# Kernel tuning notes

Hardware: AMD Instinct MI355X
Metric: run time of the kernel (lower is better)

The kernel has to match this reference:

```python
import jax, jax.numpy as jnp
import numpy as np

K = 16            # number of instance labels (static; labels are 0..K-1)
DELTA_V = 0.2     # delta_variance_loss
DELTA_D = 0.2     # delta_cluster_distance
ALPHA, BETA, GAMMA = 1.0, 1.0, 0.001


def _safe_sqrt(x):
    # sqrt with zero (not nan) gradient at x == 0
    pos = x > 0
    return jnp.where(pos, jnp.sqrt(jnp.where(pos, x, 1.0)), 0.0)


def setup_inputs() -> dict:
    key = jax.random.key(0)
    k1, k2 = jax.random.split(key)
    features = jax.random.normal(k1, (4, 32, 256, 512), dtype=jnp.float32)
    ground_truth = jax.random.randint(k2, (4, 256, 512), 0, K, dtype=jnp.int64)
    return {"features": features, "ground_truth": ground_truth}


def reference(features, ground_truth):
    N, C, H, W = features.shape
    P = H * W
    feat = features.reshape(N, C, P)                  # (N,C,P)
    gt = ground_truth.reshape(N, P)                   # (N,P)
    onehot = (gt[:, :, None] == jnp.arange(K)[None, None, :]).astype(feat.dtype)  # (N,P,K)

    # cluster mean: torch.mean(feature * mask, dim=1) -> masked sum / (H*W)  (faithful quirk)
    mu = jnp.einsum('ncp,npk->nck', feat, onehot) / P  # (N,C,K)

    # ---- variance loss ----
    # per pixel p, instance k: || feat[:,p]*mask_pk - mu[:,k] ||_2 over channels.
    # expand: mask*(||f||^2 - 2 f.mu) + ||mu||^2   (mask in {0,1} so mask^2 = mask)
    sq_f = jnp.sum(feat * feat, axis=1)               # (N,P)
    dot = jnp.einsum('ncp,nck->npk', feat, mu)        # (N,P,K)
    sq_mu = jnp.sum(mu * mu, axis=1)                  # (N,K)
    sq = onehot * (sq_f[:, :, None] - 2.0 * dot) + sq_mu[:, None, :]  # (N,P,K)
    d = _safe_sqrt(jnp.maximum(sq, 0.0))
    v = jnp.mean(d, axis=1)                           # (N,K) mean over pixels
    variance_loss = jnp.mean(jnp.mean(jnp.maximum(v - DELTA_V, 0.0), axis=1))

    # ---- distance loss ----
    gram = jnp.einsum('nck,ncj->nkj', mu, mu)         # (N,K,K)
    sqd = sq_mu[:, :, None] + sq_mu[:, None, :] - 2.0 * gram
    eye = jnp.eye(K, dtype=bool)
    D = jnp.where(eye, 0.0, _safe_sqrt(jnp.maximum(jnp.where(eye, 1.0, sqd), 0.0)))
    mean_dist = jnp.sum(D, axis=2) / (K - 1)          # mean over the K-1 other clusters
    distance_loss = jnp.sum(jnp.maximum(2.0 * DELTA_D - mean_dist, 0.0)) / (N * K)

    # ---- normalization loss ----
    normalization_loss = jnp.mean(jnp.mean(_safe_sqrt(sq_mu), axis=1))

    total_loss = ALPHA * variance_loss + BETA * distance_loss + GAMMA * normalization_loss
    return total_loss, variance_loss, distance_loss, normalization_loss, mu
```

## Files before the change

kernel.cpp:

```cpp
#include <hip/hip_runtime.h>
#include <hip/hip_bf16.h>

#define NIMG 4
#define CCH  32
#define PPIX 131072
#define KLBL 16

#define K1_CHUNK 8192
#define K1_NCHUNK (PPIX / K1_CHUNK)
#define K2_CHUNK 1024
#define K2_NCHUNK (PPIX / K2_CHUNK)

__device__ __forceinline__ float wave_sum(float v) {
#pragma unroll
    for (int m = 1; m < 64; m <<= 1) v += __shfl_xor(v, m);
    return v;
}

__global__ __launch_bounds__(256) void k1_mu(const float* __restrict__ feat,
                                             const int* __restrict__ gt,
                                             float* __restrict__ mu_raw) {
    int b     = blockIdx.x;
    int chunk = b % K1_NCHUNK;
    int cpair = (b / K1_NCHUNK) % (CCH / 2);
    int n     = b / (K1_NCHUNK * (CCH / 2));
    int c0    = cpair * 2;
    int p0    = chunk * K1_CHUNK;
    int tid   = threadIdx.x;

    const float* f0 = feat + ((size_t)(n * CCH + c0)) * PPIX + p0;
    const float* f1 = f0 + PPIX;
    const int*   g  = gt + (size_t)n * PPIX + p0;

    float acc0[KLBL], acc1[KLBL];
#pragma unroll
    for (int k = 0; k < KLBL; k++) { acc0[k] = 0.f; acc1[k] = 0.f; }

    for (int i = tid * 4; i < K1_CHUNK; i += 256 * 4) {
        float4 a  = *(const float4*)(f0 + i);
        float4 bb = *(const float4*)(f1 + i);
        int4   l  = *(const int4*)(g + i);
#pragma unroll
        for (int k = 0; k < KLBL; k++) {
            float mx = (l.x == k) ? 1.f : 0.f;
            float my = (l.y == k) ? 1.f : 0.f;
            float mz = (l.z == k) ? 1.f : 0.f;
            float mw = (l.w == k) ? 1.f : 0.f;
            acc0[k] = fmaf(a.x,  mx, acc0[k]);  acc1[k] = fmaf(bb.x, mx, acc1[k]);
            acc0[k] = fmaf(a.y,  my, acc0[k]);  acc1[k] = fmaf(bb.y, my, acc1[k]);
            acc0[k] = fmaf(a.z,  mz, acc0[k]);  acc1[k] = fmaf(bb.z, mz, acc1[k]);
            acc0[k] = fmaf(a.w,  mw, acc0[k]);  acc1[k] = fmaf(bb.w, mw, acc1[k]);
        }
    }

    __shared__ float warr[4][32];
    int wave = tid >> 6, lane = tid & 63;
#pragma unroll
    for (int k = 0; k < KLBL; k++) {
        float s0 = wave_sum(acc0[k]);
        float s1 = wave_sum(acc1[k]);
        if (lane == 0) { warr[wave][k] = s0; warr[wave][16 + k] = s1; }
    }
    __syncthreads();
    if (tid < 32) {
        float t = warr[0][tid] + warr[1][tid] + warr[2][tid] + warr[3][tid];
        int ch = tid >> 4, k = tid & 15;
        atomicAdd(&mu_raw[(n * CCH + c0 + ch) * KLBL + k], t);
    }
}

__global__ __launch_bounds__(256) void k2_var(const float* __restrict__ feat,
                                              const int* __restrict__ gt,
                                              const float* __restrict__ mu_raw,
                                              float* __restrict__ sumd,
                                              float* __restrict__ cnt) {
    __shared__ float lmu[CCH * KLBL];
    int b     = blockIdx.x;
    int chunk = b % K2_NCHUNK;
    int n     = b / K2_NCHUNK;
    int p0    = chunk * K2_CHUNK;
    int tid   = threadIdx.x;

    const float inv_p = 1.0f / (float)PPIX;
#pragma unroll
    for (int i = tid; i < CCH * KLBL; i += 256)
        lmu[i] = mu_raw[n * CCH * KLBL + i] * inv_p;
    __syncthreads();

    int p = p0 + tid * 4;
    int4 l = *(const int4*)(gt + (size_t)n * PPIX + p);
    float d2x = 0.f, d2y = 0.f, d2z = 0.f, d2w = 0.f;
    const float* fb = feat + (size_t)n * CCH * PPIX + p;
#pragma unroll 8
    for (int c = 0; c < CCH; c++) {
        float4 f = *(const float4*)(fb + (size_t)c * PPIX);
        float mx = lmu[c * KLBL + l.x];
        float my = lmu[c * KLBL + l.y];
        float mz = lmu[c * KLBL + l.z];
        float mw = lmu[c * KLBL + l.w];
        float ex = f.x - mx, ey = f.y - my, ez = f.z - mz, ew = f.w - mw;
        d2x = fmaf(ex, ex, d2x); d2y = fmaf(ey, ey, d2y);
        d2z = fmaf(ez, ez, d2z); d2w = fmaf(ew, ew, d2w);
    }
    float dx = sqrtf(d2x), dy = sqrtf(d2y), dz = sqrtf(d2z), dw = sqrtf(d2w);

    float s[KLBL], ct[KLBL];
#pragma unroll
    for (int k = 0; k < KLBL; k++) {
        float mx = (l.x == k) ? 1.f : 0.f;
        float my = (l.y == k) ? 1.f : 0.f;
        float mz = (l.z == k) ? 1.f : 0.f;
        float mw = (l.w == k) ? 1.f : 0.f;
        s[k]  = fmaf(dx, mx, fmaf(dy, my, fmaf(dz, mz, dw * mw)));
        ct[k] = mx + my + mz + mw;
    }

    __shared__ float warr[4][32];
    int wave = tid >> 6, lane = tid & 63;
#pragma unroll
    for (int k = 0; k < KLBL; k++) {
        float ssum = wave_sum(s[k]);
        float csum = wave_sum(ct[k]);
        if (lane == 0) { warr[wave][k] = ssum; warr[wave][16 + k] = csum; }
    }
    __syncthreads();
    if (tid < 32) {
        float t = warr[0][tid] + warr[1][tid] + warr[2][tid] + warr[3][tid];
        if (tid < 16) atomicAdd(&sumd[n * KLBL + tid], t);
        else          atomicAdd(&cnt[n * KLBL + (tid - 16)], t);
    }
}

__global__ __launch_bounds__(256) void k3_final(const float* __restrict__ mu_raw,
                                                const float* __restrict__ sumd,
                                                const float* __restrict__ cnt,
                                                float* __restrict__ out) {
    __shared__ float mu[NIMG * CCH * KLBL];
    __shared__ float sqmu[NIMG * KLBL];
    int t = threadIdx.x;
    const float inv_p = 1.0f / (float)PPIX;
    for (int i = t; i < NIMG * CCH * KLBL; i += 256) {
        float m = mu_raw[i] * inv_p;
        mu[i]   = m;
        out[4 + i] = m;
    }
    __syncthreads();

    float sq = 0.f;
    if (t < 64) {
        int n = t >> 4, k = t & 15;
#pragma unroll
        for (int c = 0; c < CCH; c++) {
            float m = mu[(n * CCH + c) * KLBL + k];
            sq = fmaf(m, m, sq);
        }
        sqmu[t] = sq;
    }
    __syncthreads();

    if (t < 64) {
        int n = t >> 4, k = t & 15;
        float dsum = 0.f;
#pragma unroll
        for (int j = 0; j < KLBL; j++) {
            if (j == k) continue;
            float gram = 0.f;
#pragma unroll
            for (int c = 0; c < CCH; c++)
                gram = fmaf(mu[(n * CCH + c) * KLBL + k], mu[(n * CCH + c) * KLBL + j], gram);
            float sqd = sq + sqmu[n * KLBL + j] - 2.f * gram;
            dsum += (sqd > 0.f) ? sqrtf(sqd) : 0.f;
        }
        float dist_term = fmaxf(2.f * 0.2f - dsum * (1.f / (KLBL - 1)), 0.f);
        float sqm = (sq > 0.f) ? sqrtf(sq) : 0.f;
        float v = (sumd[t] + ((float)PPIX - cnt[t]) * sqm) * inv_p;
        float var_term = fmaxf(v - 0.2f, 0.f);

        float d_r = wave_sum(dist_term);
        float v_r = wave_sum(var_term);
        float n_r = wave_sum(sqm);
        if (t == 0) {
            float variance_loss      = v_r * (1.f / (NIMG * KLBL));
            float distance_loss      = d_r * (1.f / (NIMG * KLBL));
            float normalization_loss = n_r * (1.f / (NIMG * KLBL));
            out[0] = variance_loss + distance_loss + 0.001f * normalization_loss;
            out[1] = variance_loss;
            out[2] = distance_loss;
            out[3] = normalization_loss;
        }
    }
}

extern "C" void kernel_launch(void* const* d_in, const int* in_sizes, int n_in,
                              void* d_out, int out_size, void* d_ws, size_t ws_size,
                              hipStream_t stream) {
    const float* feat = (const float*)d_in[0];
    const int*   gt   = (const int*)d_in[1];
    float* out    = (float*)d_out;
    float* mu_raw = (float*)d_ws;
    float* sumd   = mu_raw + NIMG * CCH * KLBL;
    float* cntp   = sumd + NIMG * KLBL;

    hipMemsetAsync(d_ws, 0, (NIMG * CCH * KLBL + 2 * NIMG * KLBL) * sizeof(float), stream);

    k1_mu<<<NIMG * (CCH / 2) * K1_NCHUNK, 256, 0, stream>>>(feat, gt, mu_raw);
    k2_var<<<NIMG * K2_NCHUNK, 256, 0, stream>>>(feat, gt, mu_raw, sumd, cntp);
    k3_final<<<1, 256, 0, stream>>>(mu_raw, sumd, cntp, out);
}
```

Before: 128.2 us.

## Process four channels per block and replace atomics with partial buffers

The mean kernel now handles four channels per block instead of two, which halves how often the label array is reloaded and halves the block count. Global atomics and the workspace memset are replaced by per-block partial sums written to distinct slots. The consuming kernels reduce those partials: k2 sums 16 chunk partials per mu entry in every block, and k3 reduces the variance partials. This removes the memset launch and atomic contention, but k1 uses more registers (64 accumulators) and adds redundant partial-reduction reads in k2.

After: 130.8 us. No clear change (+2.0%).

```diff
diff --git a/kernel.cpp b/kernel.cpp
--- a/kernel.cpp
+++ b/kernel.cpp
@@ -6,11 +6,14 @@
 #define PPIX 131072
 #define KLBL 16
 
+#define CPB  4
+#define NCG  (CCH / CPB)
 #define K1_CHUNK 8192
 #define K1_NCHUNK (PPIX / K1_CHUNK)
 #define K2_CHUNK 1024
 #define K2_NCHUNK (PPIX / K2_CHUNK)
 
+
 __device__ __forceinline__ float wave_sum(float v) {
 #pragma unroll
     for (int m = 1; m < 64; m <<= 1) v += __shfl_xor(v, m);
@@ -19,26 +22,29 @@
 
 __global__ __launch_bounds__(256) void k1_mu(const float* __restrict__ feat,
                                              const int* __restrict__ gt,
-                                             float* __restrict__ mu_raw) {
+                                             float* __restrict__ mu_part) {
     int b     = blockIdx.x;
     int chunk = b % K1_NCHUNK;
-    int cpair = (b / K1_NCHUNK) % (CCH / 2);
-    int n     = b / (K1_NCHUNK * (CCH / 2));
-    int c0    = cpair * 2;
+    int cg    = (b / K1_NCHUNK) % NCG;
+    int n     = b / (K1_NCHUNK * NCG);
     int p0    = chunk * K1_CHUNK;
     int tid   = threadIdx.x;
 
-    const float* f0 = feat + ((size_t)(n * CCH + c0)) * PPIX + p0;
+    const float* f0 = feat + ((size_t)(n * CCH + cg * CPB)) * PPIX + p0;
     const float* f1 = f0 + PPIX;
+    const float* f2 = f0 + 2 * (size_t)PPIX;
+    const float* f3 = f0 + 3 * (size_t)PPIX;
     const int*   g  = gt + (size_t)n * PPIX + p0;
 
-    float acc0[KLBL], acc1[KLBL];
-#pragma unroll
-    for (int k = 0; k < KLBL; k++) { acc0[k] = 0.f; acc1[k] = 0.f; }
+    float acc0[KLBL], acc1[KLBL], acc2[KLBL], acc3[KLBL];
+#pragma unroll
+    for (int k = 0; k < KLBL; k++) { acc0[k] = 0.f; acc1[k] = 0.f; acc2[k] = 0.f; acc3[k] = 0.f; }
 
     for (int i = tid * 4; i < K1_CHUNK; i += 256 * 4) {
-        float4 a  = *(const float4*)(f0 + i);
-        float4 bb = *(const float4*)(f1 + i);
+        float4 a0 = *(const float4*)(f0 + i);
+        float4 a1 = *(const float4*)(f1 + i);
+        float4 a2 = *(const float4*)(f2 + i);
+        float4 a3 = *(const float4*)(f3 + i);
         int4   l  = *(const int4*)(g + i);
 #pragma unroll
         for (int k = 0; k < KLBL; k++) {
@@ -46,45 +52,59 @@
             float my = (l.y == k) ? 1.f : 0.f;
             float mz = (l.z == k) ? 1.f : 0.f;
             float mw = (l.w == k) ? 1.f : 0.f;
-            acc0[k] = fmaf(a.x,  mx, acc0[k]);  acc1[k] = fmaf(bb.x, mx, acc1[k]);
-            acc0[k] = fmaf(a.y,  my, acc0[k]);  acc1[k] = fmaf(bb.y, my, acc1[k]);
-            acc0[k] = fmaf(a.z,  mz, acc0[k]);  acc1[k] = fmaf(bb.z, mz, acc1[k]);
-            acc0[k] = fmaf(a.w,  mw, acc0[k]);  acc1[k] = fmaf(bb.w, mw, acc1[k]);
-        }
-    }
-
-    __shared__ float warr[4][32];
+            acc0[k] = fmaf(a0.x, mx, acc0[k]); acc0[k] = fmaf(a0.y, my, acc0[k]);
+            acc0[k] = fmaf(a0.z, mz, acc0[k]); acc0[k] = fmaf(a0.w, mw, acc0[k]);
+            acc1[k] = fmaf(a1.x, mx, acc1[k]); acc1[k] = fmaf(a1.y, my, acc1[k]);
+            acc1[k] = fmaf(a1.z, mz, acc1[k]); acc1[k] = fmaf(a1.w, mw, acc1[k]);
+            acc2[k] = fmaf(a2.x, mx, acc2[k]); acc2[k] = fmaf(a2.y, my, acc2[k]);
+            acc2[k] = fmaf(a2.z, mz, acc2[k]); acc2[k] = fmaf(a2.w, mw, acc2[k]);
+            acc3[k] = fmaf(a3.x, mx, acc3[k]); acc3[k] = fmaf(a3.y, my, acc3[k]);
+            acc3[k] = fmaf(a3.z, mz, acc3[k]); acc3[k] = fmaf(a3.w, mw, acc3[k]);
+        }
+    }
+
+    __shared__ float warr[4][64];
     int wave = tid >> 6, lane = tid & 63;
 #pragma unroll
     for (int k = 0; k < KLBL; k++) {
         float s0 = wave_sum(acc0[k]);
         float s1 = wave_sum(acc1[k]);
-        if (lane == 0) { warr[wave][k] = s0; warr[wave][16 + k] = s1; }
-    }
-    __syncthreads();
-    if (tid < 32) {
+        float s2 = wave_sum(acc2[k]);
+        float s3 = wave_sum(acc3[k]);
+        if (lane == 0) {
+            warr[wave][k]      = s0;
+            warr[wave][16 + k] = s1;
+            warr[wave][32 + k] = s2;
+            warr[wave][48 + k] = s3;
+        }
+    }
+    __syncthreads();
+    if (tid < 64) {
         float t = warr[0][tid] + warr[1][tid] + warr[2][tid] + warr[3][tid];
-        int ch = tid >> 4, k = tid & 15;
-        atomicAdd(&mu_raw[(n * CCH + c0 + ch) * KLBL + k], t);
+        mu_part[(((size_t)n * K1_NCHUNK + chunk) * NCG + cg) * 64 + tid] = t;
     }
 }
 
 __global__ __launch_bounds__(256) void k2_var(const float* __restrict__ feat,
                                               const int* __restrict__ gt,
-                                              const float* __restrict__ mu_raw,
-                                              float* __restrict__ sumd,
-                                              float* __restrict__ cnt) {
+                                              const float* __restrict__ mu_part,
+                                              float* __restrict__ sumd_part,
+                                              float* __restrict__ cnt_part) {
     __shared__ float lmu[CCH * KLBL];
     int b     = blockIdx.x;
     int chunk = b % K2_NCHUNK;
     int n     = b / K2_NCHUNK;
     int p0    = chunk * K2_CHUNK;
     int tid   = threadIdx.x;
-
     const float inv_p = 1.0f / (float)PPIX;
-#pragma unroll
-    for (int i = tid; i < CCH * KLBL; i += 256)
-        lmu[i] = mu_raw[n * CCH * KLBL + i] * inv_p;
+
+    for (int e = tid; e < CCH * KLBL; e += 256) {
+        float s = 0.f;
+#pragma unroll
+        for (int ch = 0; ch < K1_NCHUNK; ch++)
+            s += mu_part[(((size_t)n * K1_NCHUNK + ch) * NCG + (e >> 6)) * 64 + (e & 63)];
+        lmu[e] = s * inv_p;
+    }
     __syncthreads();
 
     int p = p0 + tid * 4;
@@ -126,23 +146,30 @@
     __syncthreads();
     if (tid < 32) {
         float t = warr[0][tid] + warr[1][tid] + warr[2][tid] + warr[3][tid];
-        if (tid < 16) atomicAdd(&sumd[n * KLBL + tid], t);
-        else          atomicAdd(&cnt[n * KLBL + (tid - 16)], t);
-    }
-}
-
-__global__ __launch_bounds__(256) void k3_final(const float* __restrict__ mu_raw,
-                                                const float* __restrict__ sumd,
-                                                const float* __restrict__ cnt,
+        if (tid < 16) sumd_part[(size_t)b * 16 + tid]        = t;
+        else          cnt_part [(size_t)b * 16 + (tid - 16)] = t;
+    }
+}
+
+__global__ __launch_bounds__(256) void k3_final(const float* __restrict__ mu_part,
+                                                const float* __restrict__ sumd_part,
+                                                const float* __restrict__ cnt_part,
                                                 float* __restrict__ out) {
     __shared__ float mu[NIMG * CCH * KLBL];
     __shared__ float sqmu[NIMG * KLBL];
+    __shared__ float ps[4][64], pc[4][64];
     int t = threadIdx.x;
     const float inv_p = 1.0f / (float)PPIX;
-    for (int i = t; i < NIMG * CCH * KLBL; i += 256) {
-        float m = mu_raw[i] * inv_p;
-        mu[i]   = m;
-        out[4 + i] = m;
+
+    for (int m = t; m < NIMG * CCH * KLBL; m += 256) {
+        int n = m >> 9, e = m & 511;
+        float s = 0.f;
+#pragma unroll
+        for (int ch = 0; ch < K1_NCHUNK; ch++)
+            s += mu_part[(((size_t)n * K1_NCHUNK + ch) * NCG + (e >> 6)) * 64 + (e & 63)];
+        float v = s * inv_p;
+        mu[m]      = v;
+        out[4 + m] = v;
     }
     __syncthreads();
 
@@ -151,15 +178,30 @@
         int n = t >> 4, k = t & 15;
 #pragma unroll
         for (int c = 0; c < CCH; c++) {
-            float m = mu[(n * CCH + c) * KLBL + k];
+            float m = mu[n * 512 + c * KLBL + k];
             sq = fmaf(m, m, sq);
         }
         sqmu[t] = sq;
+    }
+    {
+        int q = t >> 6, nk = t & 63;
+        int n2 = nk >> 4, k2 = nk & 15;
+        float ss = 0.f, cc = 0.f;
+        for (int ch = q * 32; ch < q * 32 + 32; ch++) {
+            int idx = (n2 * K2_NCHUNK + ch) * 16 + k2;
+            ss += sumd_part[idx];
+            cc += cnt_part[idx];
+        }
+        ps[q][nk] = ss;
+        pc[q][nk] = cc;
     }
     __syncthreads();
 
     if (t < 64) {
         int n = t >> 4, k = t & 15;
+        float sumd_t = ps[0][t] + ps[1][t] + ps[2][t] + ps[3][t];
+        float cnt_t  = pc[0][t] + pc[1][t] + pc[2][t] + pc[3][t];
+
         float dsum = 0.f;
 #pragma unroll
         for (int j = 0; j < KLBL; j++) {
@@ -167,13 +209,13 @@
             float gram = 0.f;
 #pragma unroll
             for (int c = 0; c < CCH; c++)
-                gram = fmaf(mu[(n * CCH + c) * KLBL + k], mu[(n * CCH + c) * KLBL + j], gram);
+                gram = fmaf(mu[n * 512 + c * KLBL + k], mu[n * 512 + c * KLBL + j], gram);
             float sqd = sq + sqmu[n * KLBL + j] - 2.f * gram;
             dsum += (sqd > 0.f) ? sqrtf(sqd) : 0.f;
         }
         float dist_term = fmaxf(2.f * 0.2f - dsum * (1.f / (KLBL - 1)), 0.f);
         float sqm = (sq > 0.f) ? sqrtf(sq) : 0.f;
-        float v = (sumd[t] + ((float)PPIX - cnt[t]) * sqm) * inv_p;
+        float v = (sumd_t + ((float)PPIX - cnt_t) * sqm) * inv_p;
         float var_term = fmaxf(v - 0.2f, 0.f);
 
         float d_r = wave_sum(dist_term);
@@ -196,14 +238,12 @@
                               hipStream_t stream) {
     const float* feat = (const float*)d_in[0];
     const int*   gt   = (const int*)d_in[1];
-    float* out    = (float*)d_out;
-    float* mu_raw = (float*)d_ws;
-    float* sumd   = mu_raw + NIMG * CCH * KLBL;
-    float* cntp   = sumd + NIMG * KLBL;
-
-    hipMemsetAsync(d_ws, 0, (NIMG * CCH * KLBL + 2 * NIMG * KLBL) * sizeof(float), stream);
-
-    k1_mu<<<NIMG * (CCH / 2) * K1_NCHUNK, 256, 0, stream>>>(feat, gt, mu_raw);
-    k2_var<<<NIMG * K2_NCHUNK, 256, 0, stream>>>(feat, gt, mu_raw, sumd, cntp);
-    k3_final<<<1, 256, 0, stream>>>(mu_raw, sumd, cntp, out);
-}
+    float* out       = (float*)d_out;
+    float* mu_part   = (float*)d_ws;
+    float* sumd_part = mu_part + NIMG * K1_NCHUNK * NCG * 64;
+    float* cnt_part  = sumd_part + NIMG * K2_NCHUNK * 16;
+
+    k1_mu<<<NIMG * NCG * K1_NCHUNK, 256, 0, stream>>>(feat, gt, mu_part);
+    k2_var<<<NIMG * K2_NCHUNK, 256, 0, stream>>>(feat, gt, mu_part, sumd_part, cnt_part);
+    k3_final<<<1, 256, 0, stream>>>(mu_part, sumd_part, cnt_part, out);
+}
```
